# Performance work log

Hardware: AMD Instinct MI355X
Metric: run time of the kernel (lower is better)

## Reference

```python
import jax, jax.numpy as jnp
import numpy as np

N_EMBED = 1024
HEAD_SIZE = 64
BLOCK_SIZE = 4096


def setup_inputs() -> dict:
    key = jax.random.key(0)
    ks = jax.random.split(key, 7)
    s = 1.0 / np.sqrt(N_EMBED)
    return {
        "batch_x": jax.random.normal(ks[0], (4, 4096, N_EMBED), dtype=jnp.float32),
        "Wk": jax.random.uniform(ks[1], (N_EMBED, HEAD_SIZE), jnp.float32, -s, s),
        "bk": jax.random.uniform(ks[2], (HEAD_SIZE,), jnp.float32, -s, s),
        "Wq": jax.random.uniform(ks[3], (N_EMBED, HEAD_SIZE), jnp.float32, -s, s),
        "bq": jax.random.uniform(ks[4], (HEAD_SIZE,), jnp.float32, -s, s),
        "Wv": jax.random.uniform(ks[5], (N_EMBED, HEAD_SIZE), jnp.float32, -s, s),
        "bv": jax.random.uniform(ks[6], (HEAD_SIZE,), jnp.float32, -s, s),
    }


def reference(batch_x, Wk, bk, Wq, bq, Wv, bv):
    # batch_x: [B, T, C]
    T = batch_x.shape[1]
    keys = batch_x @ Wk + bk      # [B, T, H]
    queries = batch_x @ Wq + bq   # [B, T, H]
    values = batch_x @ Wv + bv    # [B, T, H]
    scale = 1.0 / jnp.sqrt(jnp.asarray(HEAD_SIZE, batch_x.dtype))
    wei = jnp.einsum("bqh,bkh->bqk", queries, keys) * scale  # [B, T, T]
    causal = jnp.tril(jnp.ones((T, T), dtype=bool))
    wei = jnp.where(causal, wei, -jnp.inf)
    wei = jax.nn.softmax(wei, axis=-1)
    out = jnp.einsum("bqk,bkh->bqh", wei, values)  # [B, T, H]
    return out
```

## Files before the change

### kernel.cpp

```cpp
#include <hip/hip_runtime.h>


using bf16x8 = __attribute__((ext_vector_type(8))) short;
using bf16x4 = __attribute__((ext_vector_type(4))) short;
using f32x4  = __attribute__((ext_vector_type(4))) float;

#define QSCALE 0.1803368867f

__device__ __forceinline__ unsigned short f2bf(float f) {
  union { float f; unsigned int u; } v; v.f = f;
  unsigned int r = v.u + 0x7fffu + ((v.u >> 16) & 1u);
  return (unsigned short)(r >> 16);
}

__device__ __forceinline__ float fexp2(float x) {
#if __has_builtin(__builtin_amdgcn_exp2f)
  return __builtin_amdgcn_exp2f(x);
#else
  float r; asm("v_exp_f32 %0, %1" : "=v"(r) : "v"(x)); return r;
#endif
}

__device__ __forceinline__ void gl_lds16(const void* g, void* l) {
  __builtin_amdgcn_global_load_lds(
      (const __attribute__((address_space(1))) void*)g,
      (__attribute__((address_space(3))) void*)l, 16, 0, 0);
}

__device__ __forceinline__ f32x4 mfma16(bf16x4 a, bf16x4 b, f32x4 c) {
#if __has_builtin(__builtin_amdgcn_mfma_f32_16x16x16bf16_1k)
  return __builtin_amdgcn_mfma_f32_16x16x16bf16_1k(a, b, c, 0, 0, 0);
#else
  f32x4 d;
  asm volatile("v_mfma_f32_16x16x16_bf16 %0, %1, %2, %3"
               : "=v"(d) : "v"(a), "v"(b), "v"(c));
  return d;
#endif
}

__global__ __launch_bounds__(256) void prep_w_kernel(
    const float* __restrict__ Wk, const float* __restrict__ Wq,
    const float* __restrict__ Wv, unsigned short* __restrict__ Wt) {
  int j = blockIdx.x;
  const float* src = (j < 64) ? Wk : ((j < 128) ? Wq : Wv);
  int jj = j & 63;
  #pragma unroll
  for (int p = 0; p < 4; ++p) {
    int k = threadIdx.x + p * 256;
    Wt[j * 1024 + k] = f2bf(src[k * 64 + jj]);
  }
}

__global__ __launch_bounds__(512) void proj8_kernel(
    const float* __restrict__ X, const unsigned short* __restrict__ Wt,
    const float* __restrict__ bk, const float* __restrict__ bq,
    const float* __restrict__ bv, unsigned short* __restrict__ Kr,
    unsigned short* __restrict__ Qs, unsigned short* __restrict__ Vt) {
  __shared__ __align__(16) float          Xl[2][32 * 64];
  __shared__ __align__(16) unsigned short Wl[2][192 * 64];
  const int tid = threadIdx.x;
  const int m0  = blockIdx.x * 32;
  const int w   = tid >> 6;
  const int mt  = w & 1;
  const int nh  = w >> 1;
  const int ln  = tid & 63;
  const int l15 = ln & 15;
  const int l4  = ln >> 4;
  const f32x4 zero4 = {0.f, 0.f, 0.f, 0.f};

  const int xr = tid >> 4, xc = tid & 15;
  const size_t xsrcLane = (size_t)(m0 + xr) * 4096 + ((xc ^ (xr & 7)) << 4);
  const char* Xb = (const char*)X;
  const char* Wb = (const char*)Wt;

  f32x4 acc[3];
  #pragma unroll
  for (int i = 0; i < 3; ++i) acc[i] = zero4;

  auto stageX = [&](int buf, int kb) {
    gl_lds16(Xb + xsrcLane + kb * 256, (char*)&Xl[buf][0] + tid * 16);
  };
  auto stageW = [&](int buf, int kb) {
    #pragma unroll
    for (int s = 0; s < 3; ++s) {
      int g = tid + s * 512;
      int row = g >> 3, gc = g & 7;
      gl_lds16(Wb + (size_t)row * 2048 + kb * 128 + ((gc ^ (row & 7)) << 4),
               (char*)&Wl[buf][0] + g * 16);
    }
  };

  stageX(0, 0);
  stageW(0, 0);
  asm volatile("s_waitcnt vmcnt(0)" ::: "memory");
  __syncthreads();

  const int rr = mt * 16 + l15;
  const int rs7 = rr & 7;
  for (int kb = 0; kb < 16; ++kb) {
    const int buf = kb & 1;
    if (kb + 1 < 16) {
      stageX(buf ^ 1, kb + 1);
      stageW(buf ^ 1, kb + 1);
    }
    const float* xp = &Xl[buf][0] + rr * 64;
    f32x4 xa0 = *reinterpret_cast<const f32x4*>(xp + (((2 * l4)     ^ rs7) << 2));
    f32x4 xa1 = *reinterpret_cast<const f32x4*>(xp + (((2 * l4 + 1) ^ rs7) << 2));
    f32x4 xb0 = *reinterpret_cast<const f32x4*>(xp + (((8 + 2 * l4) ^ rs7) << 2));
    f32x4 xb1 = *reinterpret_cast<const f32x4*>(xp + (((9 + 2 * l4) ^ rs7) << 2));
    bf16x8 a0, a1;
    #pragma unroll
    for (int i = 0; i < 4; ++i) {
      a0[i] = (short)f2bf(xa0[i]); a0[4 + i] = (short)f2bf(xa1[i]);
      a1[i] = (short)f2bf(xb0[i]); a1[4 + i] = (short)f2bf(xb1[i]);
    }
    #pragma unroll
    for (int i = 0; i < 3; ++i) {
      const int row = nh * 48 + i * 16 + l15;
      const unsigned short* wp = &Wl[buf][0] + row * 64;
      bf16x8 b0 = *reinterpret_cast<const bf16x8*>(wp + ((l4       ^ (row & 7)) << 3));
      bf16x8 b1 = *reinterpret_cast<const bf16x8*>(wp + (((4 + l4) ^ (row & 7)) << 3));
      acc[i] = __builtin_amdgcn_mfma_f32_16x16x32_bf16(a0, b0, acc[i], 0, 0, 0);
      acc[i] = __builtin_amdgcn_mfma_f32_16x16x32_bf16(a1, b1, acc[i], 0, 0, 0);
    }
    if (kb + 1 < 16) __syncthreads();
  }

  #pragma unroll
  for (int i = 0; i < 3; ++i) {
    int j = nh * 48 + i * 16 + l15;
    int mr0 = m0 + mt * 16 + l4 * 4;
    if (j < 64) {
      #pragma unroll
      for (int r = 0; r < 4; ++r)
        Kr[(size_t)(mr0 + r) * 64 + j] = f2bf(acc[i][r] + bk[j]);
    } else if (j < 128) {
      int jq = j - 64;
      #pragma unroll
      for (int r = 0; r < 4; ++r)
        Qs[(size_t)(mr0 + r) * 64 + jq] = f2bf((acc[i][r] + bq[jq]) * QSCALE);
    } else {
      int h = j - 128;
      int bb = mr0 >> 12, t0 = mr0 & 4095;
      ushort4 o;
      o.x = f2bf(acc[i][0] + bv[h]); o.y = f2bf(acc[i][1] + bv[h]);
      o.z = f2bf(acc[i][2] + bv[h]); o.w = f2bf(acc[i][3] + bv[h]);
      *reinterpret_cast<ushort4*>(&Vt[((size_t)(bb * 64 + h)) * 4096 + t0]) = o;
    }
  }
}

__global__ __launch_bounds__(512) void attn8_kernel(
    const unsigned short* __restrict__ Qs,
    const unsigned short* __restrict__ Kr,
    const unsigned short* __restrict__ Vt,
    float* __restrict__ out) {
  __shared__ __align__(16) char smem[98304];
  const int tid = threadIdx.x;
  const int w   = tid >> 6;
  const int ln  = tid & 63;
  const int l15 = ln & 15;
  const int l4  = ln >> 4;
  const int bid = blockIdx.x;
  const int pr  = bid >> 2;
  const int b   = bid & 3;
  const f32x4 zero4 = {0.f, 0.f, 0.f, 0.f};

  char* Kl = smem + w * 12288;
  char* Vl = Kl + 8192;

  const int kLane = (ln >> 3) * 128 + ((ln & 7) ^ (ln >> 3)) * 16;
  const int vLane = (ln >> 2) * 8192 + (((ln & 3) ^ ((ln >> 3) & 3))) * 16;
  const char* Kbase = (const char*)Kr + (size_t)b * 4096 * 128;
  const char* Vbase = (const char*)Vt + (size_t)b * 64 * 8192;

  auto phase = [&](int qt, bool entryBar) {
    if (entryBar) __syncthreads();
    const int qbase  = qt * 32;
    const int ntiles = qt + 1;

    const unsigned short* Q0 = Qs + ((size_t)b * 4096 + qbase + l15) * 64;
    const bf16x8 qa0 = *reinterpret_cast<const bf16x8*>(Q0 + l4 * 8);
    const bf16x8 qa1 = *reinterpret_cast<const bf16x8*>(Q0 + 32 + l4 * 8);
    const bf16x8 qb0 = *reinterpret_cast<const bf16x8*>(Q0 + 1024 + l4 * 8);
    const bf16x8 qb1 = *reinterpret_cast<const bf16x8*>(Q0 + 1024 + 32 + l4 * 8);

    f32x4 accA[4], accB[4];
    #pragma unroll
    for (int i = 0; i < 4; ++i) { accA[i] = zero4; accB[i] = zero4; }
    float mA = -1e30f, lA = 0.f, mB = -1e30f, lB = 0.f;

    auto stageK = [&](int buf, int t) {
      const char* src = Kbase + (size_t)t * 4096;
      char* dst = Kl + buf * 4096;
      #pragma unroll
      for (int c = 0; c < 4; ++c)
        gl_lds16(src + c * 1024 + kLane, dst + c * 1024 + ln * 16);
    };
    auto stageV = [&](int t) {
      const char* src = Vbase + (size_t)t * 64;
      #pragma unroll
      for (int c = 0; c < 4; ++c)
        gl_lds16(src + (size_t)c * 16 * 8192 + vLane, Vl + c * 1024 + ln * 16);
    };

    int cur = 0;
    if (w < ntiles) stageK(0, w);

    for (int t = w; t < ntiles; t += 8) {
      stageV(t);
      const bool hn = (t + 8 < ntiles);
      if (hn) stageK(cur ^ 1, t + 8);

      if (hn) asm volatile("s_waitcnt vmcnt(8)" ::: "memory");
      else    asm volatile("s_waitcnt vmcnt(4)" ::: "memory");
      __builtin_amdgcn_sched_barrier(0);

      f32x4 sA[2], sB[2];
      #pragma unroll
      for (int i = 0; i < 2; ++i) { sA[i] = zero4; sB[i] = zero4; }
      __builtin_amdgcn_s_setprio(1);
      #pragma unroll
      for (int nt = 0; nt < 2; ++nt) {
        const int krow = nt * 16 + l15;
        const unsigned short* kp =
            (const unsigned short*)(Kl + cur * 4096) + krow * 64;
        bf16x8 k0 = *reinterpret_cast<const bf16x8*>(kp + ((l4 ^ (krow & 7)) << 3));
        bf16x8 k1 = *reinterpret_cast<const bf16x8*>(kp + (((l4 + 4) ^ (krow & 7)) << 3));
        sA[nt] = __builtin_amdgcn_mfma_f32_16x16x32_bf16(k0, qa0, sA[nt], 0, 0, 0);
        sA[nt] = __builtin_amdgcn_mfma_f32_16x16x32_bf16(k1, qa1, sA[nt], 0, 0, 0);
        sB[nt] = __builtin_amdgcn_mfma_f32_16x16x32_bf16(k0, qb0, sB[nt], 0, 0, 0);
        sB[nt] = __builtin_amdgcn_mfma_f32_16x16x32_bf16(k1, qb1, sB[nt], 0, 0, 0);
      }
      __builtin_amdgcn_s_setprio(0);

      if (t == ntiles - 1) {
        const int qm = qbase + l15 - t * 32;
        #pragma unroll
        for (int nt = 0; nt < 2; ++nt)
          #pragma unroll
          for (int r = 0; r < 4; ++r) {
            int kvl = nt * 16 + 4 * l4 + r;
            if (kvl > qm)      sA[nt][r] = -1e30f;
            if (kvl > qm + 16) sB[nt][r] = -1e30f;
          }
      }

      bf16x4 paA[2], paB[2];
      {
        float x0 = fmaxf(fmaxf(sA[0][0], sA[0][1]), fmaxf(sA[0][2], sA[0][3]));
        float x1 = fmaxf(fmaxf(sA[1][0], sA[1][1]), fmaxf(sA[1][2], sA[1][3]));
        float xm = fmaxf(x0, x1);
        xm = fmaxf(xm, __shfl_xor(xm, 16));
        xm = fmaxf(xm, __shfl_xor(xm, 32));
        float mn = fmaxf(mA, xm);
        float cc = fexp2(mA - mn);
        mA = mn; lA *= cc;
        #pragma unroll
        for (int ht = 0; ht < 4; ++ht)
          #pragma unroll
          for (int r = 0; r < 4; ++r) accA[ht][r] *= cc;
        float sum = 0.f;
        #pragma unroll
        for (int nt = 0; nt < 2; ++nt) {
          #pragma unroll
          for (int r = 0; r < 4; ++r) {
            float p = fexp2(sA[nt][r] - mA);
            sA[nt][r] = p;
            paA[nt][r] = (short)f2bf(p);
          }
          sum += (sA[nt][0] + sA[nt][1]) + (sA[nt][2] + sA[nt][3]);
        }
        sum += __shfl_xor(sum, 16);
        sum += __shfl_xor(sum, 32);
        lA += sum;
      }
      {
        float x0 = fmaxf(fmaxf(sB[0][0], sB[0][1]), fmaxf(sB[0][2], sB[0][3]));
        float x1 = fmaxf(fmaxf(sB[1][0], sB[1][1]), fmaxf(sB[1][2], sB[1][3]));
        float xm = fmaxf(x0, x1);
        xm = fmaxf(xm, __shfl_xor(xm, 16));
        xm = fmaxf(xm, __shfl_xor(xm, 32));
        float mn = fmaxf(mB, xm);
        float cc = fexp2(mB - mn);
        mB = mn; lB *= cc;
        #pragma unroll
        for (int ht = 0; ht < 4; ++ht)
          #pragma unroll
          for (int r = 0; r < 4; ++r) accB[ht][r] *= cc;
        float sum = 0.f;
        #pragma unroll
        for (int nt = 0; nt < 2; ++nt) {
          #pragma unroll
          for (int r = 0; r < 4; ++r) {
            float p = fexp2(sB[nt][r] - mB);
            sB[nt][r] = p;
            paB[nt][r] = (short)f2bf(p);
          }
          sum += (sB[nt][0] + sB[nt][1]) + (sB[nt][2] + sB[nt][3]);
        }
        sum += __shfl_xor(sum, 16);
        sum += __shfl_xor(sum, 32);
        lB += sum;
      }

      if (hn) asm volatile("s_waitcnt vmcnt(4)" ::: "memory");
      else    asm volatile("s_waitcnt vmcnt(0)" ::: "memory");
      __builtin_amdgcn_sched_barrier(0);

      __builtin_amdgcn_s_setprio(1);
      #pragma unroll
      for (int nt = 0; nt < 2; ++nt) {
        #pragma unroll
        for (int ht = 0; ht < 4; ++ht) {
          const int vrow = ht * 16 + l15;
          const int g16 = (nt * 2 + (l4 >> 1)) ^ ((vrow >> 1) & 3);
          const char* vp = Vl + vrow * 64 + (g16 << 4) + ((l4 & 1) << 3);
          bf16x4 vf = *reinterpret_cast<const bf16x4*>(vp);
          accA[ht] = mfma16(vf, paA[nt], accA[ht]);
          accB[ht] = mfma16(vf, paB[nt], accB[ht]);
        }
      }
      __builtin_amdgcn_s_setprio(0);
      cur ^= 1;
    }

    __syncthreads();
    float* MO = (float*)smem;
    float* ML = (float*)(smem + 8 * 2 * 16 * 68 * 4);
    #pragma unroll
    for (int ht = 0; ht < 4; ++ht) {
      *reinterpret_cast<f32x4*>(&MO[((w * 2 + 0) * 16 + l15) * 68 + ht * 16 + 4 * l4]) = accA[ht];
      *reinterpret_cast<f32x4*>(&MO[((w * 2 + 1) * 16 + l15) * 68 + ht * 16 + 4 * l4]) = accB[ht];
    }
    if (l4 == 0) {
      ML[((w * 2 + 0) * 2 + 0) * 16 + l15] = mA;
      ML[((w * 2 + 0) * 2 + 1) * 16 + l15] = lA;
      ML[((w * 2 + 1) * 2 + 0) * 16 + l15] = mB;
      ML[((w * 2 + 1) * 2 + 1) * 16 + l15] = lB;
    }
    __syncthreads();
    {
      const int hf = tid >> 8;
      const int q  = (tid >> 4) & 15;
      const int hq = tid & 15;
      float mv[8], lv[8];
      float mM = -1e30f;
      #pragma unroll
      for (int p = 0; p < 8; ++p) {
        mv[p] = ML[((p * 2 + hf) * 2 + 0) * 16 + q];
        lv[p] = ML[((p * 2 + hf) * 2 + 1) * 16 + q];
        mM = fmaxf(mM, mv[p]);
      }
      float lT = 0.f, a[8];
      #pragma unroll
      for (int p = 0; p < 8; ++p) { a[p] = fexp2(mv[p] - mM); lT += lv[p] * a[p]; }
      float linv = 1.0f / lT;
      f32x4 o = zero4;
      #pragma unroll
      for (int p = 0; p < 8; ++p) {
        f32x4 v = *reinterpret_cast<const f32x4*>(
            &MO[((p * 2 + hf) * 16 + q) * 68 + hq * 4]);
        o[0] += v[0] * a[p]; o[1] += v[1] * a[p];
        o[2] += v[2] * a[p]; o[3] += v[3] * a[p];
      }
      float4 ov;
      ov.x = o[0] * linv; ov.y = o[1] * linv;
      ov.z = o[2] * linv; ov.w = o[3] * linv;
      *reinterpret_cast<float4*>(
          out + ((size_t)b * 4096 + qbase + hf * 16 + q) * 64 + hq * 4) = ov;
    }
  };

  phase(127 - pr, false);
  phase(pr, true);
}

template <bool WRITE_Q>
__global__ __launch_bounds__(256) void proj_kernel(
    const float* __restrict__ X,  const float* __restrict__ Wk,
    const float* __restrict__ Wq, const float* __restrict__ Wv,
    const float* __restrict__ bk, const float* __restrict__ bq,
    const float* __restrict__ bv, unsigned short* __restrict__ Kr,
    unsigned short* __restrict__ Qs, unsigned short* __restrict__ Vt) {
  constexpr int NT = WRITE_Q ? 12 : 8;
  constexpr int NC = NT / 4;
  __shared__ __align__(16) unsigned short Xl[64 * 72];
  __shared__ __align__(16) unsigned short Wl[NT * 16 * 72];
  const int tid = threadIdx.x;
  const int m0  = blockIdx.x * 64;
  const int w   = tid >> 6;
  const int ln  = tid & 63;
  const int l15 = ln & 15;
  const int l4  = ln >> 4;
  const f32x4 zero4 = {0.f, 0.f, 0.f, 0.f};
  f32x4 acc[NT];
  #pragma unroll
  for (int i = 0; i < NT; ++i) acc[i] = zero4;
  const int wn = tid & 63;
  const int wk = (tid >> 6) * 16;
  for (int kb = 0; kb < 16; ++kb) {
    __syncthreads();
    #pragma unroll
    for (int p = 0; p < 4; ++p) {
      int chunk = tid + p * 256;
      int r = chunk >> 4, c4 = chunk & 15;
      const float4 xv = *reinterpret_cast<const float4*>(
          X + (size_t)(m0 + r) * 1024 + kb * 64 + c4 * 4);
      bf16x4 o;
      o[0] = (short)f2bf(xv.x); o[1] = (short)f2bf(xv.y);
      o[2] = (short)f2bf(xv.z); o[3] = (short)f2bf(xv.w);
      *reinterpret_cast<bf16x4*>(&Xl[r * 72 + c4 * 4]) = o;
    }
    #pragma unroll
    for (int c = 0; c < NC; ++c) {
      const float* Wsrc = (c == 0) ? Wk : ((WRITE_Q && c == 1) ? Wq : Wv);
      bf16x8 w0, w1;
      #pragma unroll
      for (int j = 0; j < 8; ++j)
        w0[j] = (short)f2bf(Wsrc[(size_t)(kb * 64 + wk + j) * 64 + wn]);
      #pragma unroll
      for (int j = 0; j < 8; ++j)
        w1[j] = (short)f2bf(Wsrc[(size_t)(kb * 64 + wk + 8 + j) * 64 + wn]);
      *reinterpret_cast<bf16x8*>(&Wl[(c * 64 + wn) * 72 + wk])     = w0;
      *reinterpret_cast<bf16x8*>(&Wl[(c * 64 + wn) * 72 + wk + 8]) = w1;
    }
    __syncthreads();
    bf16x8 a0 = *reinterpret_cast<const bf16x8*>(&Xl[(w * 16 + l15) * 72 + l4 * 8]);
    bf16x8 a1 = *reinterpret_cast<const bf16x8*>(&Xl[(w * 16 + l15) * 72 + 32 + l4 * 8]);
    #pragma unroll
    for (int nt = 0; nt < NT; ++nt) {
      bf16x8 b0 = *reinterpret_cast<const bf16x8*>(&Wl[(nt * 16 + l15) * 72 + l4 * 8]);
      bf16x8 b1 = *reinterpret_cast<const bf16x8*>(&Wl[(nt * 16 + l15) * 72 + 32 + l4 * 8]);
      acc[nt] = __builtin_amdgcn_mfma_f32_16x16x32_bf16(a0, b0, acc[nt], 0, 0, 0);
      acc[nt] = __builtin_amdgcn_mfma_f32_16x16x32_bf16(a1, b1, acc[nt], 0, 0, 0);
    }
  }
  #pragma unroll
  for (int nt = 0; nt < NT; ++nt) {
    int j = nt * 16 + l15;
    #pragma unroll
    for (int r = 0; r < 4; ++r) {
      int m = m0 + w * 16 + l4 * 4 + r;
      float v = acc[nt][r];
      if (nt < 4) {
        Kr[(size_t)m * 64 + j] = f2bf(v + bk[j]);
      } else if (WRITE_Q && nt < 8) {
        Qs[(size_t)m * 64 + (j - 64)] = f2bf((v + bq[j - 64]) * QSCALE);
      } else {
        int h = j - (WRITE_Q ? 128 : 64);
        int bb = m >> 12, t = m & 4095;
        Vt[((size_t)(bb * 64 + h)) * 4096 + t] = f2bf(v + bv[h]);
      }
    }
  }
}

__global__ __launch_bounds__(256) void attnB_kernel(
    const unsigned short* __restrict__ Kr,
    const unsigned short* __restrict__ Vt,
    const float* __restrict__ X, const float* __restrict__ Wq,
    const float* __restrict__ bq, float* __restrict__ out) {
  __shared__ __align__(16) unsigned short Kl[64 * 72];
  __shared__ __align__(16) unsigned short Vl[64 * 72];
  __shared__ __align__(16) unsigned short Pl[4 * 16 * 72];
  const int tid = threadIdx.x;
  const int w   = tid >> 6;
  const int ln  = tid & 63;
  const int l15 = ln & 15;
  const int l4  = ln >> 4;
  const int b   = blockIdx.y;
  const int q0  = blockIdx.x * 64;
  const int qrow = q0 + w * 16;
  const f32x4 zero4 = {0.f, 0.f, 0.f, 0.f};
  unsigned short* Pw = &Pl[w * 16 * 72];
  f32x4 accq[4];
  #pragma unroll
  for (int i = 0; i < 4; ++i) accq[i] = zero4;
  const int wn = tid & 63;
  const int wk = (tid >> 6) * 16;
  for (int kb = 0; kb < 16; ++kb) {
    __syncthreads();
    #pragma unroll
    for (int p = 0; p < 4; ++p) {
      int chunk = tid + p * 256;
      int r = chunk >> 4, c4 = chunk & 15;
      const float4 xv = *reinterpret_cast<const float4*>(
          X + ((size_t)b * 4096 + q0 + r) * 1024 + kb * 64 + c4 * 4);
      bf16x4 o;
      o[0] = (short)f2bf(xv.x); o[1] = (short)f2bf(xv.y);
      o[2] = (short)f2bf(xv.z); o[3] = (short)f2bf(xv.w);
      *reinterpret_cast<bf16x4*>(&Kl[r * 72 + c4 * 4]) = o;
    }
    bf16x8 w0, w1;
    #pragma unroll
    for (int j = 0; j < 8; ++j)
      w0[j] = (short)f2bf(Wq[(size_t)(kb * 64 + wk + j) * 64 + wn]);
    #pragma unroll
    for (int j = 0; j < 8; ++j)
      w1[j] = (short)f2bf(Wq[(size_t)(kb * 64 + wk + 8 + j) * 64 + wn]);
    *reinterpret_cast<bf16x8*>(&Vl[wn * 72 + wk])     = w0;
    *reinterpret_cast<bf16x8*>(&Vl[wn * 72 + wk + 8]) = w1;
    __syncthreads();
    bf16x8 a0 = *reinterpret_cast<const bf16x8*>(&Kl[(w * 16 + l15) * 72 + l4 * 8]);
    bf16x8 a1 = *reinterpret_cast<const bf16x8*>(&Kl[(w * 16 + l15) * 72 + 32 + l4 * 8]);
    #pragma unroll
    for (int nt = 0; nt < 4; ++nt) {
      bf16x8 b0 = *reinterpret_cast<const bf16x8*>(&Vl[(nt * 16 + l15) * 72 + l4 * 8]);
      bf16x8 b1 = *reinterpret_cast<const bf16x8*>(&Vl[(nt * 16 + l15) * 72 + 32 + l4 * 8]);
      accq[nt] = __builtin_amdgcn_mfma_f32_16x16x32_bf16(a0, b0, accq[nt], 0, 0, 0);
      accq[nt] = __builtin_amdgcn_mfma_f32_16x16x32_bf16(a1, b1, accq[nt], 0, 0, 0);
    }
  }
  #pragma unroll
  for (int nt = 0; nt < 4; ++nt) {
    int h = nt * 16 + l15;
    #pragma unroll
    for (int r = 0; r < 4; ++r)
      Pw[(l4 * 4 + r) * 72 + h] = f2bf((accq[nt][r] + bq[h]) * 0.125f);
  }
  asm volatile("s_waitcnt lgkmcnt(0)" ::: "memory");
  __builtin_amdgcn_sched_barrier(0);
  bf16x8 qa0 = *reinterpret_cast<const bf16x8*>(&Pw[l15 * 72 + l4 * 8]);
  bf16x8 qa1 = *reinterpret_cast<const bf16x8*>(&Pw[l15 * 72 + 32 + l4 * 8]);
  f32x4 acco[4];
  #pragma unroll
  for (int i = 0; i < 4; ++i) acco[i] = zero4;
  float mrow[4] = {-1e30f, -1e30f, -1e30f, -1e30f};
  float lrow[4] = {0.f, 0.f, 0.f, 0.f};
  const int ktmax = blockIdx.x;
  for (int kt = 0; kt <= ktmax; ++kt) {
    const int kv0 = kt * 64;
    __syncthreads();
    #pragma unroll
    for (int p = 0; p < 2; ++p) {
      int chunk = tid + p * 256;
      int r = chunk >> 3, c8 = chunk & 7;
      *reinterpret_cast<bf16x8*>(&Kl[r * 72 + c8 * 8]) =
          *reinterpret_cast<const bf16x8*>(Kr + ((size_t)b * 4096 + kv0 + r) * 64 + c8 * 8);
      *reinterpret_cast<bf16x8*>(&Vl[r * 72 + c8 * 8]) =
          *reinterpret_cast<const bf16x8*>(Vt + ((size_t)b * 64 + r) * 4096 + kv0 + c8 * 8);
    }
    __syncthreads();
    f32x4 s[4];
    #pragma unroll
    for (int i = 0; i < 4; ++i) s[i] = zero4;
    #pragma unroll
    for (int nt = 0; nt < 4; ++nt) {
      bf16x8 k0 = *reinterpret_cast<const bf16x8*>(&Kl[(nt * 16 + l15) * 72 + l4 * 8]);
      bf16x8 k1 = *reinterpret_cast<const bf16x8*>(&Kl[(nt * 16 + l15) * 72 + 32 + l4 * 8]);
      s[nt] = __builtin_amdgcn_mfma_f32_16x16x32_bf16(qa0, k0, s[nt], 0, 0, 0);
      s[nt] = __builtin_amdgcn_mfma_f32_16x16x32_bf16(qa1, k1, s[nt], 0, 0, 0);
    }
    if (kt == ktmax) {
      #pragma unroll
      for (int nt = 0; nt < 4; ++nt) {
        int kv_g = kv0 + nt * 16 + l15;
        #pragma unroll
        for (int r = 0; r < 4; ++r) {
          int q_g = qrow + l4 * 4 + r;
          if (kv_g > q_g) s[nt][r] = -1e30f;
        }
      }
    }
    #pragma unroll
    for (int r = 0; r < 4; ++r) {
      float t = fmaxf(fmaxf(s[0][r], s[1][r]), fmaxf(s[2][r], s[3][r]));
      t = fmaxf(t, __shfl_xor(t, 1));
      t = fmaxf(t, __shfl_xor(t, 2));
      t = fmaxf(t, __shfl_xor(t, 4));
      t = fmaxf(t, __shfl_xor(t, 8));
      float mnew = fmaxf(mrow[r], t);
      float cc = __expf(mrow[r] - mnew);
      mrow[r] = mnew;
      lrow[r] *= cc;
      acco[0][r] *= cc; acco[1][r] *= cc; acco[2][r] *= cc; acco[3][r] *= cc;
    }
    #pragma unroll
    for (int nt = 0; nt < 4; ++nt) {
      #pragma unroll
      for (int r = 0; r < 4; ++r) {
        float p = __expf(s[nt][r] - mrow[r]);
        s[nt][r] = p;
        Pw[(l4 * 4 + r) * 72 + nt * 16 + l15] = f2bf(p);
      }
    }
    #pragma unroll
    for (int r = 0; r < 4; ++r) {
      float t = s[0][r] + s[1][r] + s[2][r] + s[3][r];
      t += __shfl_xor(t, 1);
      t += __shfl_xor(t, 2);
      t += __shfl_xor(t, 4);
      t += __shfl_xor(t, 8);
      lrow[r] += t;
    }
    asm volatile("s_waitcnt lgkmcnt(0)" ::: "memory");
    __builtin_amdgcn_sched_barrier(0);
    #pragma unroll
    for (int ks = 0; ks < 2; ++ks) {
      bf16x8 pa = *reinterpret_cast<const bf16x8*>(&Pw[l15 * 72 + ks * 32 + l4 * 8]);
      #pragma unroll
      for (int ht = 0; ht < 4; ++ht) {
        bf16x8 vf = *reinterpret_cast<const bf16x8*>(&Vl[(ht * 16 + l15) * 72 + ks * 32 + l4 * 8]);
        acco[ht] = __builtin_amdgcn_mfma_f32_16x16x32_bf16(pa, vf, acco[ht], 0, 0, 0);
      }
    }
  }
  float* ob = out + ((size_t)b * 4096 + qrow) * 64;
  #pragma unroll
  for (int ht = 0; ht < 4; ++ht) {
    #pragma unroll
    for (int r = 0; r < 4; ++r) {
      ob[(l4 * 4 + r) * 64 + ht * 16 + l15] = acco[ht][r] / lrow[r];
    }
  }
}

extern "C" void kernel_launch(void* const* d_in, const int* in_sizes, int n_in,
                              void* d_out, int out_size, void* d_ws, size_t ws_size,
                              hipStream_t stream) {
  const float* X  = (const float*)d_in[0];
  const float* Wk = (const float*)d_in[1];
  const float* bk = (const float*)d_in[2];
  const float* Wq = (const float*)d_in[3];
  const float* bq = (const float*)d_in[4];
  const float* Wv = (const float*)d_in[5];
  const float* bv = (const float*)d_in[6];
  float* out = (float*)d_out;

  char* ws = (char*)d_ws;
  const size_t SZ = 2097152;
  const size_t WT = 393216;
  unsigned short* Kr = (unsigned short*)(ws);
  unsigned short* Vt = (unsigned short*)(ws + SZ);

  if (ws_size >= 3 * SZ) {
    unsigned short* Qs = (unsigned short*)(ws + 2 * SZ);
    unsigned short* Wt = (ws_size >= 3 * SZ + WT)
                             ? (unsigned short*)(ws + 3 * SZ)
                             : (unsigned short*)d_out;
    prep_w_kernel<<<192, 256, 0, stream>>>(Wk, Wq, Wv, Wt);
    proj8_kernel<<<512, 512, 0, stream>>>(X, Wt, bk, bq, bv, Kr, Qs, Vt);
    attn8_kernel<<<256, 512, 0, stream>>>(Qs, Kr, Vt, out);
  } else {
    proj_kernel<false><<<256, 256, 0, stream>>>(X, Wk, Wq, Wv, bk, bq, bv, Kr, nullptr, Vt);
    attnB_kernel<<<dim3(64, 4), 256, 0, stream>>>(Kr, Vt, X, Wq, bq, out);
  }
}
```

Before: 58.19 us.

## Split projection into smaller 16-row by 64-column blocks for more parallelism

The fused QKV projection kernel now runs 3072 blocks of 256 threads, each computing 16 rows by one 64-column slice (K, Q or V), in place of 512 blocks of 512 threads that each computed 32 rows by all 192 columns. The aim is more blocks to spread across CUs and smaller per-block LDS to improve occupancy. In exchange, each X tile (fp32) is now loaded and converted to bf16 three times, once per column chunk, which triples X global reads, the largest input at 64MB.

```diff
diff --git a/kernel.cpp b/kernel.cpp
--- a/kernel.cpp
+++ b/kernel.cpp
@@ -51,18 +51,19 @@
   }
 }
 
-__global__ __launch_bounds__(512) void proj8_kernel(
+__global__ __launch_bounds__(256) void proj10_kernel(
     const float* __restrict__ X, const unsigned short* __restrict__ Wt,
     const float* __restrict__ bk, const float* __restrict__ bq,
     const float* __restrict__ bv, unsigned short* __restrict__ Kr,
     unsigned short* __restrict__ Qs, unsigned short* __restrict__ Vt) {
-  __shared__ __align__(16) float          Xl[2][32 * 64];
-  __shared__ __align__(16) unsigned short Wl[2][192 * 64];
+  __shared__ __align__(16) float          Xl[2][16 * 64];
+  __shared__ __align__(16) unsigned short Wl[2][64 * 64];
   const int tid = threadIdx.x;
-  const int m0  = blockIdx.x * 32;
+  const int bid = blockIdx.x;
+  const int mt  = bid / 3;
+  const int nc  = bid % 3;
+  const int m0  = mt * 16;
   const int w   = tid >> 6;
-  const int mt  = w & 1;
-  const int nh  = w >> 1;
   const int ln  = tid & 63;
   const int l15 = ln & 15;
   const int l4  = ln >> 4;
@@ -71,19 +72,17 @@
   const int xr = tid >> 4, xc = tid & 15;
   const size_t xsrcLane = (size_t)(m0 + xr) * 4096 + ((xc ^ (xr & 7)) << 4);
   const char* Xb = (const char*)X;
-  const char* Wb = (const char*)Wt;
-
-  f32x4 acc[3];
-  #pragma unroll
-  for (int i = 0; i < 3; ++i) acc[i] = zero4;
+  const char* Wb = (const char*)Wt + (size_t)nc * 64 * 2048;
+
+  f32x4 acc = zero4;
 
   auto stageX = [&](int buf, int kb) {
     gl_lds16(Xb + xsrcLane + kb * 256, (char*)&Xl[buf][0] + tid * 16);
   };
   auto stageW = [&](int buf, int kb) {
     #pragma unroll
-    for (int s = 0; s < 3; ++s) {
-      int g = tid + s * 512;
+    for (int s = 0; s < 2; ++s) {
+      int g = tid + s * 256;
       int row = g >> 3, gc = g & 7;
       gl_lds16(Wb + (size_t)row * 2048 + kb * 128 + ((gc ^ (row & 7)) << 4),
                (char*)&Wl[buf][0] + g * 16);
@@ -95,8 +94,10 @@
   asm volatile("s_waitcnt vmcnt(0)" ::: "memory");
   __syncthreads();
 
-  const int rr = mt * 16 + l15;
+  const int rr  = l15;
   const int rs7 = rr & 7;
+  const int wrow = w * 16 + l15;
+  const int ws7 = wrow & 7;
   for (int kb = 0; kb < 16; ++kb) {
     const int buf = kb & 1;
     if (kb + 1 < 16) {
@@ -114,39 +115,32 @@
       a0[i] = (short)f2bf(xa0[i]); a0[4 + i] = (short)f2bf(xa1[i]);
       a1[i] = (short)f2bf(xb0[i]); a1[4 + i] = (short)f2bf(xb1[i]);
     }
-    #pragma unroll
-    for (int i = 0; i < 3; ++i) {
-      const int row = nh * 48 + i * 16 + l15;
-      const unsigned short* wp = &Wl[buf][0] + row * 64;
-      bf16x8 b0 = *reinterpret_cast<const bf16x8*>(wp + ((l4       ^ (row & 7)) << 3));
-      bf16x8 b1 = *reinterpret_cast<const bf16x8*>(wp + (((4 + l4) ^ (row & 7)) << 3));
-      acc[i] = __builtin_amdgcn_mfma_f32_16x16x32_bf16(a0, b0, acc[i], 0, 0, 0);
-      acc[i] = __builtin_amdgcn_mfma_f32_16x16x32_bf16(a1, b1, acc[i], 0, 0, 0);
-    }
+    const unsigned short* wp = &Wl[buf][0] + wrow * 64;
+    bf16x8 b0 = *reinterpret_cast<const bf16x8*>(wp + ((l4       ^ ws7) << 3));
+    bf16x8 b1 = *reinterpret_cast<const bf16x8*>(wp + (((4 + l4) ^ ws7) << 3));
+    acc = __builtin_amdgcn_mfma_f32_16x16x32_bf16(a0, b0, acc, 0, 0, 0);
+    acc = __builtin_amdgcn_mfma_f32_16x16x32_bf16(a1, b1, acc, 0, 0, 0);
     if (kb + 1 < 16) __syncthreads();
   }
 
-  #pragma unroll
-  for (int i = 0; i < 3; ++i) {
-    int j = nh * 48 + i * 16 + l15;
-    int mr0 = m0 + mt * 16 + l4 * 4;
-    if (j < 64) {
-      #pragma unroll
-      for (int r = 0; r < 4; ++r)
-        Kr[(size_t)(mr0 + r) * 64 + j] = f2bf(acc[i][r] + bk[j]);
-    } else if (j < 128) {
-      int jq = j - 64;
-      #pragma unroll
-      for (int r = 0; r < 4; ++r)
-        Qs[(size_t)(mr0 + r) * 64 + jq] = f2bf((acc[i][r] + bq[jq]) * QSCALE);
-    } else {
-      int h = j - 128;
-      int bb = mr0 >> 12, t0 = mr0 & 4095;
-      ushort4 o;
-      o.x = f2bf(acc[i][0] + bv[h]); o.y = f2bf(acc[i][1] + bv[h]);
-      o.z = f2bf(acc[i][2] + bv[h]); o.w = f2bf(acc[i][3] + bv[h]);
-      *reinterpret_cast<ushort4*>(&Vt[((size_t)(bb * 64 + h)) * 4096 + t0]) = o;
-    }
+  const int j   = nc * 64 + w * 16 + l15;
+  const int mr0 = m0 + l4 * 4;
+  if (j < 64) {
+    #pragma unroll
+    for (int r = 0; r < 4; ++r)
+      Kr[(size_t)(mr0 + r) * 64 + j] = f2bf(acc[r] + bk[j]);
+  } else if (j < 128) {
+    int jq = j - 64;
+    #pragma unroll
+    for (int r = 0; r < 4; ++r)
+      Qs[(size_t)(mr0 + r) * 64 + jq] = f2bf((acc[r] + bq[jq]) * QSCALE);
+  } else {
+    int h = j - 128;
+    int bb = mr0 >> 12, t0 = mr0 & 4095;
+    ushort4 o;
+    o.x = f2bf(acc[0] + bv[h]); o.y = f2bf(acc[1] + bv[h]);
+    o.z = f2bf(acc[2] + bv[h]); o.w = f2bf(acc[3] + bv[h]);
+    *reinterpret_cast<ushort4*>(&Vt[((size_t)(bb * 64 + h)) * 4096 + t0]) = o;
   }
 }
 
@@ -640,7 +634,7 @@
                              ? (unsigned short*)(ws + 3 * SZ)
                              : (unsigned short*)d_out;
     prep_w_kernel<<<192, 256, 0, stream>>>(Wk, Wq, Wv, Wt);
-    proj8_kernel<<<512, 512, 0, stream>>>(X, Wt, bk, bq, bv, Kr, Qs, Vt);
+    proj10_kernel<<<3072, 256, 0, stream>>>(X, Wt, bk, bq, bv, Kr, Qs, Vt);
     attn8_kernel<<<256, 512, 0, stream>>>(Qs, Kr, Vt, out);
   } else {
     proj_kernel<false><<<256, 256, 0, stream>>>(X, Wk, Wq, Wv, bk, bq, bv, Kr, nullptr, Vt);
```

After: 78.81 us. 35.4% more time.

## Restructure projection to keep a column slice of W resident in LDS

Applied to the files above, without the earlier changes.

The projection kernel now splits the 192 output columns into four chunks of 48. Each block loads its whole bf16 W slice (96KB) into LDS once and covers 128 rows. Each wave streams its own 16 rows of X through a private triple buffer, using vmcnt waits instead of block-wide barriers. This removes the per-k-step block syncs and the repeated W staging, but each X row is now read by four different blocks. That extra X traffic depends on L2/MALL hits, and the large LDS allocation allows only one block per CU.

```diff
diff --git a/kernel.cpp b/kernel.cpp
--- a/kernel.cpp
+++ b/kernel.cpp
@@ -51,85 +51,86 @@
   }
 }
 
-__global__ __launch_bounds__(512) void proj8_kernel(
+__global__ __launch_bounds__(512) void proj15_kernel(
     const float* __restrict__ X, const unsigned short* __restrict__ Wt,
     const float* __restrict__ bk, const float* __restrict__ bq,
     const float* __restrict__ bv, unsigned short* __restrict__ Kr,
     unsigned short* __restrict__ Qs, unsigned short* __restrict__ Vt) {
-  __shared__ __align__(16) float          Xl[2][32 * 64];
-  __shared__ __align__(16) unsigned short Wl[2][192 * 64];
+  __shared__ __align__(16) char smem[147456];
   const int tid = threadIdx.x;
-  const int m0  = blockIdx.x * 32;
+  const int bid = blockIdx.x;
+  const int mtb = bid & 127;
+  const int nc  = bid >> 7;
   const int w   = tid >> 6;
-  const int mt  = w & 1;
-  const int nh  = w >> 1;
   const int ln  = tid & 63;
   const int l15 = ln & 15;
   const int l4  = ln >> 4;
+  const int m0w = mtb * 128 + w * 16;
   const f32x4 zero4 = {0.f, 0.f, 0.f, 0.f};
 
-  const int xr = tid >> 4, xc = tid & 15;
-  const size_t xsrcLane = (size_t)(m0 + xr) * 4096 + ((xc ^ (xr & 7)) << 4);
-  const char* Xb = (const char*)X;
-  const char* Wb = (const char*)Wt;
-
-  f32x4 acc[3];
-  #pragma unroll
-  for (int i = 0; i < 3; ++i) acc[i] = zero4;
-
-  auto stageX = [&](int buf, int kb) {
-    gl_lds16(Xb + xsrcLane + kb * 256, (char*)&Xl[buf][0] + tid * 16);
+  char* Wl = smem;
+  char* Xb = smem + 98304 + w * 6144;
+
+  {
+    const char* Wbase = (const char*)Wt + (size_t)nc * 48 * 2048;
+    #pragma unroll
+    for (int s = 0; s < 12; ++s) {
+      int g = tid + s * 512;
+      int row = g >> 7, slot = g & 127;
+      gl_lds16(Wbase + (size_t)row * 2048 + ((slot ^ (row & 7)) << 4),
+               Wl + g * 16);
+    }
+  }
+  const int xrr = (ln >> 3) & 7;
+  auto stageX = [&](int t) {
+    char* dst = Xb + (t % 3) * 2048;
+    #pragma unroll
+    for (int s = 0; s < 2; ++s) {
+      int r = 8 * s + (ln >> 3);
+      int g = ln & 7;
+      gl_lds16((const char*)X + (size_t)(m0w + r) * 4096 + t * 128 +
+                   ((g ^ (r & 7)) << 4),
+               dst + s * 1024 + ln * 16);
+    }
   };
-  auto stageW = [&](int buf, int kb) {
-    #pragma unroll
-    for (int s = 0; s < 3; ++s) {
-      int g = tid + s * 512;
-      int row = g >> 3, gc = g & 7;
-      gl_lds16(Wb + (size_t)row * 2048 + kb * 128 + ((gc ^ (row & 7)) << 4),
-               (char*)&Wl[buf][0] + g * 16);
-    }
-  };
-
-  stageX(0, 0);
-  stageW(0, 0);
+  stageX(0);
+  stageX(1);
   asm volatile("s_waitcnt vmcnt(0)" ::: "memory");
   __syncthreads();
 
-  const int rr = mt * 16 + l15;
-  const int rs7 = rr & 7;
-  for (int kb = 0; kb < 16; ++kb) {
-    const int buf = kb & 1;
-    if (kb + 1 < 16) {
-      stageX(buf ^ 1, kb + 1);
-      stageW(buf ^ 1, kb + 1);
-    }
-    const float* xp = &Xl[buf][0] + rr * 64;
-    f32x4 xa0 = *reinterpret_cast<const f32x4*>(xp + (((2 * l4)     ^ rs7) << 2));
-    f32x4 xa1 = *reinterpret_cast<const f32x4*>(xp + (((2 * l4 + 1) ^ rs7) << 2));
-    f32x4 xb0 = *reinterpret_cast<const f32x4*>(xp + (((8 + 2 * l4) ^ rs7) << 2));
-    f32x4 xb1 = *reinterpret_cast<const f32x4*>(xp + (((9 + 2 * l4) ^ rs7) << 2));
-    bf16x8 a0, a1;
+  f32x4 acc[3];
+  #pragma unroll
+  for (int i = 0; i < 3; ++i) acc[i] = zero4;
+
+  const int rs7 = l15 & 7;
+  for (int t = 0; t < 32; ++t) {
+    const bool pf = (t + 2 < 32);
+    if (pf) stageX(t + 2);
+    const char* xp = Xb + (t % 3) * 2048 + l15 * 128;
+    f32x4 xa0 = *reinterpret_cast<const f32x4*>(xp + (((2 * l4)     ^ rs7) << 4));
+    f32x4 xa1 = *reinterpret_cast<const f32x4*>(xp + (((2 * l4 + 1) ^ rs7) << 4));
+    bf16x8 a0;
     #pragma unroll
     for (int i = 0; i < 4; ++i) {
-      a0[i] = (short)f2bf(xa0[i]); a0[4 + i] = (short)f2bf(xa1[i]);
-      a1[i] = (short)f2bf(xb0[i]); a1[4 + i] = (short)f2bf(xb1[i]);
+      a0[i]     = (short)f2bf(xa0[i]);
+      a0[4 + i] = (short)f2bf(xa1[i]);
     }
     #pragma unroll
     for (int i = 0; i < 3; ++i) {
-      const int row = nh * 48 + i * 16 + l15;
-      const unsigned short* wp = &Wl[buf][0] + row * 64;
-      bf16x8 b0 = *reinterpret_cast<const bf16x8*>(wp + ((l4       ^ (row & 7)) << 3));
-      bf16x8 b1 = *reinterpret_cast<const bf16x8*>(wp + (((4 + l4) ^ (row & 7)) << 3));
+      const int j = i * 16 + l15;
+      bf16x8 b0 = *reinterpret_cast<const bf16x8*>(
+          Wl + j * 2048 + (((4 * t + l4) ^ (j & 7)) << 4));
       acc[i] = __builtin_amdgcn_mfma_f32_16x16x32_bf16(a0, b0, acc[i], 0, 0, 0);
-      acc[i] = __builtin_amdgcn_mfma_f32_16x16x32_bf16(a1, b1, acc[i], 0, 0, 0);
-    }
-    if (kb + 1 < 16) __syncthreads();
+    }
+    if (pf)           asm volatile("s_waitcnt vmcnt(2)" ::: "memory");
+    else if (t < 31)  asm volatile("s_waitcnt vmcnt(0)" ::: "memory");
+    __builtin_amdgcn_sched_barrier(0);
   }
 
   #pragma unroll
   for (int i = 0; i < 3; ++i) {
-    int j = nh * 48 + i * 16 + l15;
-    int mr0 = m0 + mt * 16 + l4 * 4;
+    int j   = nc * 48 + i * 16 + l15;
+    int mr0 = m0w + l4 * 4;
     if (j < 64) {
       #pragma unroll
       for (int r = 0; r < 4; ++r)
@@ -148,6 +149,7 @@
       *reinterpret_cast<ushort4*>(&Vt[((size_t)(bb * 64 + h)) * 4096 + t0]) = o;
     }
   }
+  (void)xrr;
 }
 
 __global__ __launch_bounds__(512) void attn8_kernel(
@@ -640,7 +642,7 @@
                              ? (unsigned short*)(ws + 3 * SZ)
                              : (unsigned short*)d_out;
     prep_w_kernel<<<192, 256, 0, stream>>>(Wk, Wq, Wv, Wt);
-    proj8_kernel<<<512, 512, 0, stream>>>(X, Wt, bk, bq, bv, Kr, Qs, Vt);
+    proj15_kernel<<<512, 512, 0, stream>>>(X, Wt, bk, bq, bv, Kr, Qs, Vt);
     attn8_kernel<<<256, 512, 0, stream>>>(Qs, Kr, Vt, out);
   } else {
     proj_kernel<false><<<256, 256, 0, stream>>>(X, Wk, Wq, Wv, bk, bq, bv, Kr, nullptr, Vt);
```

Measured after the change: 62.98 us. 8.2% more time.
